# Kernel tuning notes

Hardware: AMD Instinct MI355X
Metric: run time of the kernel (lower is better)

The kernel has to match this reference:

```python
import jax, jax.numpy as jnp
import numpy as np

B, T, D, H = 4, 1024, 1024, 16
HD = D // H
MAX_LEN = 1024


def _layernorm(x, g, b, eps=1e-5):
    mu = jnp.mean(x, axis=-1, keepdims=True)
    var = jnp.var(x, axis=-1, keepdims=True)
    return (x - mu) * jax.lax.rsqrt(var + eps) * g + b


def setup_inputs() -> dict:
    key = jax.random.key(0)
    ks = jax.random.split(key, 12)
    s = 1.0 / np.sqrt(D)
    return {
        "src": jax.random.normal(ks[0], (B, T, D), jnp.float32),
        "Wqkv": jax.random.uniform(ks[1], (D, 3 * D), jnp.float32, -s, s),
        "bqkv": jnp.zeros((3 * D,), jnp.float32),
        "Wo": jax.random.uniform(ks[2], (D, D), jnp.float32, -s, s),
        "bo": jnp.zeros((D,), jnp.float32),
        "rel_bias": 0.02 * jax.random.normal(ks[3], (H, 2 * MAX_LEN - 1), jnp.float32),
        "temperature": jnp.float32(1.0),
        "W1": jax.random.uniform(ks[4], (D, 4 * D), jnp.float32, -s, s),
        "b1": jnp.zeros((4 * D,), jnp.float32),
        "W2": jax.random.uniform(ks[5], (4 * D, D), jnp.float32, -1.0 / np.sqrt(4 * D), 1.0 / np.sqrt(4 * D)),
        "b2": jnp.zeros((D,), jnp.float32),
        "ff_scale": jnp.ones((1,), jnp.float32),
        "gamma1": jnp.ones((D,), jnp.float32),
        "beta1": jnp.zeros((D,), jnp.float32),
        "gamma2": jnp.ones((D,), jnp.float32),
        "beta2": jnp.zeros((D,), jnp.float32),
    }


def reference(src, Wqkv, bqkv, Wo, bo, rel_bias, temperature, W1, b1, W2, b2,
              ff_scale, gamma1, beta1, gamma2, beta2):
    b, t, c = src.shape
    # QKV projection -> [3, B, H, T, HD]
    qkv = (src @ Wqkv + bqkv).reshape(b, t, 3, H, HD).transpose(2, 0, 3, 1, 4)
    q, k, v = qkv[0], qkv[1], qkv[2]
    temp = jnp.maximum(temperature, 0.01)  # clamp(min=0.01)
    logits = jnp.einsum("bhqd,bhkd->bhqk", q, k) / temp
    # relative position bias gather: [H, T, T]
    pos = jnp.arange(t)
    rel = pos[None, :] - pos[:, None] + (t - 1)
    logits = logits + rel_bias[:, rel][None]
    attn_weights = jax.nn.softmax(logits, axis=-1)
    attn_out = jnp.einsum("bhqk,bhkd->bhqd", attn_weights, v)
    attn_out = attn_out.transpose(0, 2, 1, 3).reshape(b, t, c) @ Wo + bo
    x = _layernorm(src + attn_out, gamma1, beta1)
    ff = jax.nn.gelu(x @ W1 + b1, approximate=False) @ W2 + b2
    out = _layernorm(x + ff_scale * ff, gamma2, beta2)
    return (out, attn_weights)
```

## Files before the change

### kernel.cpp

```cpp
#include <hip/hip_runtime.h>
#include <math.h>

#define BB 4
#define TT 1024
#define DM 1024
#define NH 16
#define HD 64
#define DFF 4096
#define N3 3072

typedef unsigned short u16;
typedef __attribute__((ext_vector_type(4))) float f32x4;
typedef __attribute__((ext_vector_type(8))) short s16x8;

__device__ __forceinline__ u16 f2bf(float f) {
    union { float f; unsigned u; } v; v.f = f;
    unsigned u = v.u;
    u += 0x7fffu + ((u >> 16) & 1u);
    return (u16)(u >> 16);
}
__device__ __forceinline__ float bf2f(u16 h) {
    union { unsigned u; float f; } v; v.u = ((unsigned)h) << 16;
    return v.f;
}

__device__ __forceinline__ void async_copy16(const void* g, void* l) {
    __builtin_amdgcn_global_load_lds(
        (const __attribute__((address_space(1))) unsigned int*)g,
        (__attribute__((address_space(3))) unsigned int*)l, 16, 0, 0);
}

__global__ __launch_bounds__(256) void cvt_kernel(const float* __restrict__ in,
                                                  u16* __restrict__ out, int n) {
    int i = (blockIdx.x * 256 + threadIdx.x) * 4;
    if (i + 3 < n) {
        out[i + 0] = f2bf(in[i + 0]);
        out[i + 1] = f2bf(in[i + 1]);
        out[i + 2] = f2bf(in[i + 2]);
        out[i + 3] = f2bf(in[i + 3]);
    }
}

template<int TIN>
__global__ __launch_bounds__(256) void transpose_kernel(const void* __restrict__ inv,
                                                        u16* __restrict__ out, int R, int C) {
    __shared__ float tile[32][33];
    const float* inF = (const float*)inv;
    const u16* inH = (const u16*)inv;
    size_t boff = (size_t)blockIdx.z * R * C;
    int c0 = blockIdx.x * 32, r0 = blockIdx.y * 32;
    int tx = threadIdx.x & 31, ty = threadIdx.x >> 5;
    for (int i = 0; i < 4; i++) {
        int r = r0 + ty + i * 8, c = c0 + tx;
        float v = (TIN == 0) ? inF[boff + (size_t)r * C + c] : bf2f(inH[boff + (size_t)r * C + c]);
        tile[ty + i * 8][tx] = v;
    }
    __syncthreads();
    for (int i = 0; i < 4; i++) {
        int rr = r0 + tx, cc = c0 + ty + i * 8;
        out[boff + (size_t)cc * R + rr] = f2bf(tile[tx][ty + i * 8]);
    }
}

template<int EPI>
__global__ __launch_bounds__(256) void gemm_kernel(const u16* __restrict__ A,
                                                   const u16* __restrict__ BT,
                                                   const float* __restrict__ bias,
                                                   void* __restrict__ out0v,
                                                   u16* __restrict__ out1, u16* __restrict__ out2,
                                                   int M, int N, int Kstride, int Ksl) {
    __shared__ u16 As[128 * 32];
    __shared__ u16 Bs[128 * 32];
    const int tid = threadIdx.x;
    const int lane = tid & 63;
    const int wave = tid >> 6;
    const int quad = lane >> 4;
    const int l15 = lane & 15;
    const int wy = wave >> 1, wx = wave & 1;
    const int m0 = blockIdx.y * 128;
    const int n0 = blockIdx.x * 128;
    const int koff = blockIdx.z * Ksl;

    const int ai0 = wave * 2, ai1 = wave * 2 + 1;
    const u16* aG0 = A + (size_t)(m0 + ai0 * 16 + (lane >> 2)) * Kstride + (lane & 3) * 8;
    const u16* aG1 = A + (size_t)(m0 + ai1 * 16 + (lane >> 2)) * Kstride + (lane & 3) * 8;
    const u16* bG0 = BT + (size_t)(n0 + ai0 * 16 + (lane >> 2)) * Kstride + (lane & 3) * 8;
    const u16* bG1 = BT + (size_t)(n0 + ai1 * 16 + (lane >> 2)) * Kstride + (lane & 3) * 8;
    u16* aL0 = &As[ai0 * 512];
    u16* aL1 = &As[ai1 * 512];
    u16* bL0 = &Bs[ai0 * 512];
    u16* bL1 = &Bs[ai1 * 512];

    f32x4 acc[4][4] = {};

    for (int k0 = koff; k0 < koff + Ksl; k0 += 32) {
        async_copy16(aG0 + k0, aL0);
        async_copy16(aG1 + k0, aL1);
        async_copy16(bG0 + k0, bL0);
        async_copy16(bG1 + k0, bL1);
        __syncthreads();
        s16x8 af[4], bf[4];
#pragma unroll
        for (int i = 0; i < 4; i++)
            af[i] = *(const s16x8*)&As[(wy * 64 + i * 16 + l15) * 32 + quad * 8];
#pragma unroll
        for (int j = 0; j < 4; j++)
            bf[j] = *(const s16x8*)&Bs[(wx * 64 + j * 16 + l15) * 32 + quad * 8];
#pragma unroll
        for (int i = 0; i < 4; i++)
#pragma unroll
            for (int j = 0; j < 4; j++)
                acc[i][j] = __builtin_amdgcn_mfma_f32_16x16x32_bf16(af[i], bf[j], acc[i][j], 0, 0, 0);
        __syncthreads();
    }

    const size_t MN = (size_t)M * N;
#pragma unroll
    for (int i = 0; i < 4; i++) {
#pragma unroll
        for (int j = 0; j < 4; j++) {
            f32x4 c = acc[i][j];
            int gn = n0 + wx * 64 + j * 16 + l15;
            float bv = (EPI == 3) ? 0.f : bias[gn];
#pragma unroll
            for (int r = 0; r < 4; r++) {
                int gm = m0 + wy * 64 + i * 16 + quad * 4 + r;
                float v = c[r] + bv;
                if (EPI == 2) v = 0.5f * v * (1.f + erff(v * 0.70710678118f));
                if (EPI == 0 || EPI == 2) {
                    ((u16*)out0v)[(size_t)gm * N + gn] = f2bf(v);
                } else if (EPI == 3) {
                    ((float*)out0v)[(size_t)blockIdx.z * MN + (size_t)gm * N + gn] = v;
                } else {
                    int which = gn >> 10, h = (gn >> 6) & 15, d = gn & 63;
                    int bb = gm >> 10, t = gm & 1023;
                    u16* dst = (which == 0) ? (u16*)out0v : ((which == 1) ? out1 : out2);
                    dst[((size_t)(bb * NH + h) * TT + t) * HD + d] = f2bf(v);
                }
            }
        }
    }
}

__global__ __launch_bounds__(512) void attn_kernel(const u16* __restrict__ Qb,
                                                   const u16* __restrict__ Kb,
                                                   const u16* __restrict__ VTb,
                                                   const float* __restrict__ rel_bias,
                                                   const float* __restrict__ temp_p,
                                                   float* __restrict__ probs_out,
                                                   u16* __restrict__ attn_out) {
    __shared__ __align__(16) u16 Qs[16 * 72];
    __shared__ __align__(16) u16 Ps[16 * 1032];
    __shared__ float red[2][8][16];
    __shared__ float RB[1040];

    const int tid = threadIdx.x;
    const int lane = tid & 63, wave = tid >> 6, quad = lane >> 4, l15 = lane & 15;
    const int q0 = blockIdx.x * 16;
    const int h = blockIdx.y, b = blockIdx.z;
    const int bh = b * NH + h;
    const size_t headoff = (size_t)bh * TT * HD;

    float temp = fmaxf(temp_p[0], 0.01f);
    const float itemp = 1.f / temp;

    for (int i = tid; i < 1039; i += 512)
        RB[i] = rel_bias[h * 2047 + (1008 - q0) + i];
    if (tid < 256) {
        int row = tid >> 4, col = (tid & 15) * 4;
        const u16* srcp = Qb + headoff + (size_t)(q0 + row) * HD + col;
        *(uint2*)&Qs[row * 72 + col] = *(const uint2*)srcp;
    }
    __syncthreads();

    s16x8 a0 = *(const s16x8*)&Qs[l15 * 72 + quad * 8];
    s16x8 a1 = *(const s16x8*)&Qs[l15 * 72 + 32 + quad * 8];
    f32x4 s[8];
    const u16* Kh = Kb + headoff;
#pragma unroll
    for (int nt = 0; nt < 8; nt++) {
        int key = wave * 128 + nt * 16 + l15;
        const u16* kp = Kh + (size_t)key * HD;
        s16x8 b0 = *(const s16x8*)(kp + quad * 8);
        s16x8 b1 = *(const s16x8*)(kp + 32 + quad * 8);
        f32x4 acc = {};
        acc = __builtin_amdgcn_mfma_f32_16x16x32_bf16(a0, b0, acc, 0, 0, 0);
        acc = __builtin_amdgcn_mfma_f32_16x16x32_bf16(a1, b1, acc, 0, 0, 0);
#pragma unroll
        for (int r = 0; r < 4; r++)
            acc[r] = acc[r] * itemp + RB[key - (quad * 4 + r) + 15];
        s[nt] = acc;
    }

    float lm[4];
#pragma unroll
    for (int r = 0; r < 4; r++) {
        float m = s[0][r];
#pragma unroll
        for (int nt = 1; nt < 8; nt++) m = fmaxf(m, s[nt][r]);
        for (int off = 8; off >= 1; off >>= 1) m = fmaxf(m, __shfl_xor(m, off));
        lm[r] = m;
    }
    if (l15 == 0)
        for (int r = 0; r < 4; r++) red[0][wave][quad * 4 + r] = lm[r];
    __syncthreads();
    float rm[4];
#pragma unroll
    for (int r = 0; r < 4; r++) {
        int row = quad * 4 + r;
        float m = red[0][0][row];
#pragma unroll
        for (int w = 1; w < 8; w++) m = fmaxf(m, red[0][w][row]);
        rm[r] = m;
    }

    float ls[4] = {0.f, 0.f, 0.f, 0.f};
#pragma unroll
    for (int nt = 0; nt < 8; nt++)
#pragma unroll
        for (int r = 0; r < 4; r++) {
            float p = __expf(s[nt][r] - rm[r]);
            s[nt][r] = p;
            ls[r] += p;
        }
#pragma unroll
    for (int r = 0; r < 4; r++) {
        float v = ls[r];
        for (int off = 8; off >= 1; off >>= 1) v += __shfl_xor(v, off);
        ls[r] = v;
    }
    if (l15 == 0)
        for (int r = 0; r < 4; r++) red[1][wave][quad * 4 + r] = ls[r];
    __syncthreads();
    float inv[4];
#pragma unroll
    for (int r = 0; r < 4; r++) {
        int row = quad * 4 + r;
        float v = red[1][0][row];
#pragma unroll
        for (int w = 1; w < 8; w++) v += red[1][w][row];
        inv[r] = 1.f / v;
    }

    float* prow = probs_out + ((size_t)bh * TT + q0) * TT;
#pragma unroll
    for (int nt = 0; nt < 8; nt++) {
        int key = wave * 128 + nt * 16 + l15;
#pragma unroll
        for (int r = 0; r < 4; r++) {
            int row = quad * 4 + r;
            float pn = s[nt][r] * inv[r];
            prow[(size_t)row * TT + key] = pn;
            Ps[row * 1032 + key] = f2bf(pn);
        }
    }
    __syncthreads();

    f32x4 o[4] = {};
    const u16* Vh = VTb + headoff;
#pragma unroll
    for (int ks = 0; ks < 4; ks++) {
        int k0 = wave * 128 + ks * 32;
        s16x8 pa = *(const s16x8*)&Ps[l15 * 1032 + k0 + quad * 8];
#pragma unroll
        for (int nt = 0; nt < 4; nt++) {
            int d = nt * 16 + l15;
            s16x8 vb = *(const s16x8*)(Vh + (size_t)d * TT + k0 + quad * 8);
            o[nt] = __builtin_amdgcn_mfma_f32_16x16x32_bf16(pa, vb, o[nt], 0, 0, 0);
        }
    }
    __syncthreads();
    float* OpF = (float*)Ps;
#pragma unroll
    for (int nt = 0; nt < 4; nt++)
#pragma unroll
        for (int r = 0; r < 4; r++)
            OpF[(wave * 16 + quad * 4 + r) * 64 + nt * 16 + l15] = o[nt][r];
    __syncthreads();

    {
        int m = tid >> 5, dc = (tid & 31) * 2;
        float a0v = 0.f, a1v = 0.f;
#pragma unroll
        for (int w = 0; w < 8; w++) {
            a0v += OpF[(w * 16 + m) * 64 + dc];
            a1v += OpF[(w * 16 + m) * 64 + dc + 1];
        }
        u16 pk[2] = {f2bf(a0v), f2bf(a1v)};
        *(unsigned*)&attn_out[((size_t)(b * TT + q0 + m)) * DM + h * HD + dc] = *(unsigned*)pk;
    }
}

template<int MODE, int KS>
__global__ __launch_bounds__(256) void ln_kernel(const float* __restrict__ af32,
                                                 const u16* __restrict__ abf,
                                                 const float* __restrict__ part,
                                                 const float* __restrict__ biasN,
                                                 const float* __restrict__ scale_p,
                                                 const float* __restrict__ gamma,
                                                 const float* __restrict__ beta,
                                                 float* __restrict__ outf,
                                                 u16* __restrict__ outbf) {
    __shared__ float red[2][4];
    const size_t MN = (size_t)BB * TT * DM;
    int row = blockIdx.x;
    int tid = threadIdx.x;
    float sc = (MODE == 1) ? scale_p[0] : 1.f;
    int c0 = tid * 4;
    size_t base = (size_t)row * DM + c0;
    float4 a = *(const float4*)(biasN + c0);
    float acc[4] = {a.x, a.y, a.z, a.w};
#pragma unroll
    for (int kz = 0; kz < KS; kz++) {
        float4 p = *(const float4*)(part + kz * MN + base);
        acc[0] += p.x; acc[1] += p.y; acc[2] += p.z; acc[3] += p.w;
    }
    float x[4];
#pragma unroll
    for (int c = 0; c < 4; c++) {
        float b0 = (MODE == 0) ? af32[base + c] : bf2f(abf[base + c]);
        x[c] = b0 + sc * acc[c];
    }
    float s = x[0] + x[1] + x[2] + x[3];
    float sq = x[0] * x[0] + x[1] * x[1] + x[2] * x[2] + x[3] * x[3];
    for (int off = 32; off >= 1; off >>= 1) {
        s += __shfl_xor(s, off);
        sq += __shfl_xor(sq, off);
    }
    int wave = tid >> 6;
    if ((tid & 63) == 0) {
        red[0][wave] = s;
        red[1][wave] = sq;
    }
    __syncthreads();
    s = red[0][0] + red[0][1] + red[0][2] + red[0][3];
    sq = red[1][0] + red[1][1] + red[1][2] + red[1][3];
    float mu = s * (1.f / DM);
    float var = sq * (1.f / DM) - mu * mu;
    float rs = rsqrtf(var + 1e-5f);
#pragma unroll
    for (int c = 0; c < 4; c++) {
        float y = (x[c] - mu) * rs * gamma[c0 + c] + beta[c0 + c];
        if (MODE == 0) outbf[base + c] = f2bf(y);
        else outf[base + c] = y;
    }
}

#define OFF_SRCBF 0UL
#define OFF_WQKVT 8388608UL
#define OFF_WOT 14680064UL
#define OFF_W1T 16777216UL
#define OFF_W2T 25165824UL
#define OFF_Q 33554432UL
#define OFF_K 41943040UL
#define OFF_V 50331648UL
#define OFF_VT 58720256UL
#define OFF_ATTNO 67108864UL
#define OFF_XBF 83886080UL
#define OFF_H1 92274688UL
#define OFF_PART 134217728UL

extern "C" void kernel_launch(void* const* d_in, const int* in_sizes, int n_in,
                              void* d_out, int out_size, void* d_ws, size_t ws_size,
                              hipStream_t stream) {
    const float* src = (const float*)d_in[0];
    const float* Wqkv = (const float*)d_in[1];
    const float* bqkv = (const float*)d_in[2];
    const float* Wo = (const float*)d_in[3];
    const float* bo = (const float*)d_in[4];
    const float* relb = (const float*)d_in[5];
    const float* temp = (const float*)d_in[6];
    const float* W1 = (const float*)d_in[7];
    const float* b1 = (const float*)d_in[8];
    const float* W2 = (const float*)d_in[9];
    const float* b2 = (const float*)d_in[10];
    const float* ffs = (const float*)d_in[11];
    const float* g1 = (const float*)d_in[12];
    const float* be1 = (const float*)d_in[13];
    const float* g2 = (const float*)d_in[14];
    const float* be2 = (const float*)d_in[15];

    char* ws = (char*)d_ws;
    u16* srcbf = (u16*)(ws + OFF_SRCBF);
    u16* WqkvT = (u16*)(ws + OFF_WQKVT);
    u16* WoT = (u16*)(ws + OFF_WOT);
    u16* W1T = (u16*)(ws + OFF_W1T);
    u16* W2T = (u16*)(ws + OFF_W2T);
    u16* Qb = (u16*)(ws + OFF_Q);
    u16* Kb = (u16*)(ws + OFF_K);
    u16* Vb = (u16*)(ws + OFF_V);
    u16* VTb = (u16*)(ws + OFF_VT);
    u16* attnbf = (u16*)(ws + OFF_ATTNO);
    u16* xbf = (u16*)(ws + OFF_XBF);
    u16* h1bf = (u16*)(ws + OFF_H1);
    float* partF = (float*)(ws + OFF_PART);

    float* out_f = (float*)d_out;
    float* probs = out_f + (size_t)BB * TT * DM;

    cvt_kernel<<<4096, 256, 0, stream>>>(src, srcbf, BB * TT * DM);
    transpose_kernel<0><<<dim3(N3 / 32, DM / 32, 1), 256, 0, stream>>>(Wqkv, WqkvT, DM, N3);
    transpose_kernel<0><<<dim3(DM / 32, DM / 32, 1), 256, 0, stream>>>(Wo, WoT, DM, DM);
    transpose_kernel<0><<<dim3(DFF / 32, DM / 32, 1), 256, 0, stream>>>(W1, W1T, DM, DFF);
    transpose_kernel<0><<<dim3(DM / 32, DFF / 32, 1), 256, 0, stream>>>(W2, W2T, DFF, DM);
    gemm_kernel<1><<<dim3(N3 / 128, (BB * TT) / 128, 1), 256, 0, stream>>>(
        srcbf, WqkvT, bqkv, Qb, Kb, Vb, BB * TT, N3, DM, DM);
    transpose_kernel<1><<<dim3(HD / 32, TT / 32, BB * NH), 256, 0, stream>>>(Vb, VTb, TT, HD);
    attn_kernel<<<dim3(TT / 16, NH, BB), 512, 0, stream>>>(Qb, Kb, VTb, relb, temp, probs, attnbf);
    gemm_kernel<3><<<dim3(DM / 128, (BB * TT) / 128, 2), 256, 0, stream>>>(
        attnbf, WoT, nullptr, partF, nullptr, nullptr, BB * TT, DM, DM, DM / 2);
    ln_kernel<0, 2><<<BB * TT, 256, 0, stream>>>(src, nullptr, partF, bo, nullptr, g1, be1,
                                                 nullptr, xbf);
    gemm_kernel<2><<<dim3(DFF / 128, (BB * TT) / 128, 1), 256, 0, stream>>>(
        xbf, W1T, b1, h1bf, nullptr, nullptr, BB * TT, DFF, DM, DM);
    gemm_kernel<3><<<dim3(DM / 128, (BB * TT) / 128, 4), 256, 0, stream>>>(
        h1bf, W2T, nullptr, partF, nullptr, nullptr, BB * TT, DM, DFF, DFF / 4);
    ln_kernel<1, 4><<<BB * TT, 256, 0, stream>>>(nullptr, xbf, partF, b2, ffs, g2, be2,
                                                 out_f, nullptr);
}
```

Baseline: 707.4 us.

## Replace 128x128 GEMM with 256x256 four-stage pipelined swizzled MFMA kernel

```diff
diff --git a/kernel.cpp b/kernel.cpp
--- a/kernel.cpp
+++ b/kernel.cpp
@@ -62,80 +62,118 @@
     }
 }
 
-template<int EPI>
-__global__ __launch_bounds__(256) void gemm_kernel(const u16* __restrict__ A,
-                                                   const u16* __restrict__ BT,
-                                                   const float* __restrict__ bias,
-                                                   void* __restrict__ out0v,
-                                                   u16* __restrict__ out1, u16* __restrict__ out2,
-                                                   int M, int N, int Kstride, int Ksl) {
-    __shared__ u16 As[128 * 32];
-    __shared__ u16 Bs[128 * 32];
+template<int EPI, int NT>
+__global__ __launch_bounds__(512, 2) void gemm256_kernel(const u16* __restrict__ A,
+                                                         const u16* __restrict__ BT,
+                                                         const float* __restrict__ bias,
+                                                         void* __restrict__ out0v,
+                                                         u16* __restrict__ out1,
+                                                         u16* __restrict__ out2,
+                                                         int M, int N, int Kstride) {
+    __shared__ u16 As[4][8192];
+    __shared__ u16 Bs[4][8192];
     const int tid = threadIdx.x;
     const int lane = tid & 63;
     const int wave = tid >> 6;
     const int quad = lane >> 4;
     const int l15 = lane & 15;
-    const int wy = wave >> 1, wx = wave & 1;
-    const int m0 = blockIdx.y * 128;
-    const int n0 = blockIdx.x * 128;
-    const int koff = blockIdx.z * Ksl;
-
-    const int ai0 = wave * 2, ai1 = wave * 2 + 1;
-    const u16* aG0 = A + (size_t)(m0 + ai0 * 16 + (lane >> 2)) * Kstride + (lane & 3) * 8;
-    const u16* aG1 = A + (size_t)(m0 + ai1 * 16 + (lane >> 2)) * Kstride + (lane & 3) * 8;
-    const u16* bG0 = BT + (size_t)(n0 + ai0 * 16 + (lane >> 2)) * Kstride + (lane & 3) * 8;
-    const u16* bG1 = BT + (size_t)(n0 + ai1 * 16 + (lane >> 2)) * Kstride + (lane & 3) * 8;
-    u16* aL0 = &As[ai0 * 512];
-    u16* aL1 = &As[ai1 * 512];
-    u16* bL0 = &Bs[ai0 * 512];
-    u16* bL1 = &Bs[ai1 * 512];
-
-    f32x4 acc[4][4] = {};
-
-    for (int k0 = koff; k0 < koff + Ksl; k0 += 32) {
-        async_copy16(aG0 + k0, aL0);
-        async_copy16(aG1 + k0, aL1);
-        async_copy16(bG0 + k0, bL0);
-        async_copy16(bG1 + k0, bL1);
-        __syncthreads();
-        s16x8 af[4], bf[4];
+    const int wm = wave >> 2;
+    const int wn = wave & 3;
+    const int m0 = blockIdx.y * 256;
+    const int n0 = blockIdx.x * 256;
+    const int koff = blockIdx.z * (NT * 32);
+
+    const int srow = wave * 32 + (lane >> 2);
+    const int schunk = ((lane & 3) ^ ((lane >> 2) & 3)) * 8;
+    const u16* aG0 = A + (size_t)(m0 + srow) * Kstride + koff + schunk;
+    const u16* aG1 = aG0 + (size_t)16 * Kstride;
+    const u16* bG0 = BT + (size_t)(n0 + srow) * Kstride + koff + schunk;
+    const u16* bG1 = bG0 + (size_t)16 * Kstride;
+    const int ldst0 = wave * 1024;
+    const int ldst1 = wave * 1024 + 512;
+
+#define STAGE_A(t) { int kk_ = (t) * 32; \
+    async_copy16(aG0 + kk_, &As[(t) & 3][ldst0]); \
+    async_copy16(aG1 + kk_, &As[(t) & 3][ldst1]); }
+#define STAGE_B(t) { int kk_ = (t) * 32; \
+    async_copy16(bG0 + kk_, &Bs[(t) & 3][ldst0]); \
+    async_copy16(bG1 + kk_, &Bs[(t) & 3][ldst1]); }
+
+    const int swq = (quad ^ (l15 & 3)) * 8;
+    const int abase = (wm * 128 + l15) * 32 + swq;
+    const int bbase = (wn * 64 + l15) * 32 + swq;
+
+    f32x4 acc[8][4] = {};
+
+    STAGE_A(0); STAGE_B(0);
+    STAGE_A(1); STAGE_B(1);
+    STAGE_A(2); STAGE_B(2);
+
+#pragma unroll 1
+    for (int t = 0; t < NT; ++t) {
+        if (t < NT - 2)       asm volatile("s_waitcnt vmcnt(8)" ::: "memory");
+        else if (t == NT - 2) asm volatile("s_waitcnt vmcnt(4)" ::: "memory");
+        else                  asm volatile("s_waitcnt vmcnt(0)" ::: "memory");
+        asm volatile("" ::: "memory");
+        __builtin_amdgcn_s_barrier();
+        asm volatile("" ::: "memory");
+
+        const u16* as = As[t & 3];
+        const u16* bs = Bs[t & 3];
+
+        s16x8 bfr[4];
+#pragma unroll
+        for (int j = 0; j < 4; j++)
+            bfr[j] = *(const s16x8*)&bs[bbase + j * 512];
+        s16x8 afr[4];
 #pragma unroll
         for (int i = 0; i < 4; i++)
-            af[i] = *(const s16x8*)&As[(wy * 64 + i * 16 + l15) * 32 + quad * 8];
-#pragma unroll
-        for (int j = 0; j < 4; j++)
-            bf[j] = *(const s16x8*)&Bs[(wx * 64 + j * 16 + l15) * 32 + quad * 8];
+            afr[i] = *(const s16x8*)&as[abase + i * 512];
+        if (t + 3 < NT) STAGE_A(t + 3);
+        __builtin_amdgcn_s_setprio(1);
 #pragma unroll
         for (int i = 0; i < 4; i++)
 #pragma unroll
             for (int j = 0; j < 4; j++)
-                acc[i][j] = __builtin_amdgcn_mfma_f32_16x16x32_bf16(af[i], bf[j], acc[i][j], 0, 0, 0);
-        __syncthreads();
-    }
+                acc[i][j] = __builtin_amdgcn_mfma_f32_16x16x32_bf16(afr[i], bfr[j], acc[i][j], 0, 0, 0);
+        __builtin_amdgcn_s_setprio(0);
+#pragma unroll
+        for (int i = 0; i < 4; i++)
+            afr[i] = *(const s16x8*)&as[abase + 2048 + i * 512];
+        if (t + 3 < NT) STAGE_B(t + 3);
+        __builtin_amdgcn_s_setprio(1);
+#pragma unroll
+        for (int i = 0; i < 4; i++)
+#pragma unroll
+            for (int j = 0; j < 4; j++)
+                acc[i + 4][j] = __builtin_amdgcn_mfma_f32_16x16x32_bf16(afr[i], bfr[j], acc[i + 4][j], 0, 0, 0);
+        __builtin_amdgcn_s_setprio(0);
+    }
+#undef STAGE_A
+#undef STAGE_B
 
     const size_t MN = (size_t)M * N;
 #pragma unroll
-    for (int i = 0; i < 4; i++) {
+    for (int i = 0; i < 8; i++) {
 #pragma unroll
         for (int j = 0; j < 4; j++) {
             f32x4 c = acc[i][j];
-            int gn = n0 + wx * 64 + j * 16 + l15;
+            int gn = n0 + wn * 64 + j * 16 + l15;
             float bv = (EPI == 3) ? 0.f : bias[gn];
 #pragma unroll
             for (int r = 0; r < 4; r++) {
-                int gm = m0 + wy * 64 + i * 16 + quad * 4 + r;
+                int gm = m0 + wm * 128 + i * 16 + quad * 4 + r;
                 float v = c[r] + bv;
-                if (EPI == 2) v = 0.5f * v * (1.f + erff(v * 0.70710678118f));
-                if (EPI == 0 || EPI == 2) {
+                if (EPI == 2) {
+                    v = 0.5f * v * (1.f + erff(v * 0.70710678118f));
                     ((u16*)out0v)[(size_t)gm * N + gn] = f2bf(v);
                 } else if (EPI == 3) {
                     ((float*)out0v)[(size_t)blockIdx.z * MN + (size_t)gm * N + gn] = v;
                 } else {
                     int which = gn >> 10, h = (gn >> 6) & 15, d = gn & 63;
-                    int bb = gm >> 10, t = gm & 1023;
+                    int bb = gm >> 10, tq = gm & 1023;
                     u16* dst = (which == 0) ? (u16*)out0v : ((which == 1) ? out1 : out2);
-                    dst[((size_t)(bb * NH + h) * TT + t) * HD + d] = f2bf(v);
+                    dst[((size_t)(bb * NH + h) * TT + tq) * HD + d] = f2bf(v);
                 }
             }
         }
@@ -403,18 +441,18 @@
     transpose_kernel<0><<<dim3(DM / 32, DM / 32, 1), 256, 0, stream>>>(Wo, WoT, DM, DM);
     transpose_kernel<0><<<dim3(DFF / 32, DM / 32, 1), 256, 0, stream>>>(W1, W1T, DM, DFF);
     transpose_kernel<0><<<dim3(DM / 32, DFF / 32, 1), 256, 0, stream>>>(W2, W2T, DFF, DM);
-    gemm_kernel<1><<<dim3(N3 / 128, (BB * TT) / 128, 1), 256, 0, stream>>>(
-        srcbf, WqkvT, bqkv, Qb, Kb, Vb, BB * TT, N3, DM, DM);
+    gemm256_kernel<1, 32><<<dim3(N3 / 256, (BB * TT) / 256, 1), 512, 0, stream>>>(
+        srcbf, WqkvT, bqkv, Qb, Kb, Vb, BB * TT, N3, DM);
     transpose_kernel<1><<<dim3(HD / 32, TT / 32, BB * NH), 256, 0, stream>>>(Vb, VTb, TT, HD);
     attn_kernel<<<dim3(TT / 16, NH, BB), 512, 0, stream>>>(Qb, Kb, VTb, relb, temp, probs, attnbf);
-    gemm_kernel<3><<<dim3(DM / 128, (BB * TT) / 128, 2), 256, 0, stream>>>(
-        attnbf, WoT, nullptr, partF, nullptr, nullptr, BB * TT, DM, DM, DM / 2);
+    gemm256_kernel<3, 16><<<dim3(DM / 256, (BB * TT) / 256, 2), 512, 0, stream>>>(
+        attnbf, WoT, nullptr, partF, nullptr, nullptr, BB * TT, DM, DM);
     ln_kernel<0, 2><<<BB * TT, 256, 0, stream>>>(src, nullptr, partF, bo, nullptr, g1, be1,
                                                  nullptr, xbf);
-    gemm_kernel<2><<<dim3(DFF / 128, (BB * TT) / 128, 1), 256, 0, stream>>>(
-        xbf, W1T, b1, h1bf, nullptr, nullptr, BB * TT, DFF, DM, DM);
-    gemm_kernel<3><<<dim3(DM / 128, (BB * TT) / 128, 4), 256, 0, stream>>>(
-        h1bf, W2T, nullptr, partF, nullptr, nullptr, BB * TT, DM, DFF, DFF / 4);
+    gemm256_kernel<2, 32><<<dim3(DFF / 256, (BB * TT) / 256, 1), 512, 0, stream>>>(
+        xbf, W1T, b1, h1bf, nullptr, nullptr, BB * TT, DFF, DM);
+    gemm256_kernel<3, 32><<<dim3(DM / 256, (BB * TT) / 256, 4), 512, 0, stream>>>(
+        h1bf, W2T, nullptr, partF, nullptr, nullptr, BB * TT, DM, DFF);
     ln_kernel<1, 4><<<BB * TT, 256, 0, stream>>>(nullptr, xbf, partF, b2, ffs, g2, be2,
                                                  out_f, nullptr);
 }
```

New measurement: 658.6 us. 6.9% less time.
